# Kernel optimization log

Hardware: AMD Instinct MI355X
Metric: run time of the kernel (lower is better)

Reference implementation:

```python
import jax, jax.numpy as jnp
import numpy as np

B, C, H, W = 4, 256, 64, 64
CI = C // 2  # inter_channels


def setup_inputs() -> dict:
    key = jax.random.key(0)
    ks = jax.random.split(key, 10)
    s_in = 1.0 / np.sqrt(C)
    s_out = 1.0 / np.sqrt(CI)
    return {
        "rgbd": jax.random.normal(ks[0], (B, C, H, W), jnp.float32),
        "x": jax.random.normal(ks[1], (B, C, H, W), jnp.float32),
        "q_w": jax.random.uniform(ks[2], (CI, C), jnp.float32, -s_in, s_in),
        "q_b": jax.random.uniform(ks[3], (CI,), jnp.float32, -s_in, s_in),
        "k_w": jax.random.uniform(ks[4], (CI, C), jnp.float32, -s_in, s_in),
        "k_b": jax.random.uniform(ks[5], (CI,), jnp.float32, -s_in, s_in),
        "v_w": jax.random.uniform(ks[6], (CI, C), jnp.float32, -s_in, s_in),
        "v_b": jax.random.uniform(ks[7], (CI,), jnp.float32, -s_in, s_in),
        "out_w": jax.random.uniform(ks[8], (C, CI), jnp.float32, -s_out, s_out),
        "out_b": jax.random.uniform(ks[9], (C,), jnp.float32, -s_out, s_out),
    }


def reference(rgbd, x, q_w, q_b, k_w, k_b, v_w, v_b, out_w, out_b):
    b, c, h, w = rgbd.shape
    ci = q_w.shape[0]
    n = h * w
    # 1x1 convs == channel-wise linear maps; flatten spatial to tokens
    xs = x.reshape(b, c, n)        # [B, C, N]
    rs = rgbd.reshape(b, c, n)     # [B, C, N]
    q = jnp.einsum('oc,bcn->bno', q_w, xs) + q_b          # [B, N, CI]
    k = jnp.einsum('oc,bcn->bon', k_w, rs) + k_b[:, None]  # [B, CI, N]
    v = jnp.einsum('oc,bcn->bno', v_w, rs) + v_b          # [B, N, CI]
    attn = jax.nn.softmax(jnp.einsum('bqc,bck->bqk', q, k), axis=-1)  # [B, N, N]
    out = jnp.einsum('bqk,bkc->bqc', attn, v)             # [B, N, CI]
    out = jnp.einsum('oc,bnc->bon', out_w, out) + out_b[:, None]  # [B, C, N]
    return rgbd + out.reshape(b, c, h, w)
```

## Files before the change

### kernel.cpp

```cpp
#include <hip/hip_runtime.h>
#include <cstdint>
#include <cstddef>

typedef unsigned short u16;
typedef __attribute__((ext_vector_type(8))) short bf16x8;
typedef __attribute__((ext_vector_type(4))) float f32x4;
typedef __attribute__((ext_vector_type(16))) float f32x16;
typedef __attribute__((ext_vector_type(4))) uint32_t u32x4;

#define DEV __device__ __forceinline__

static constexpr float LOG2E = 1.4426950408889634f;

DEV u16 f2bf(float f) {
  uint32_t u = __float_as_uint(f);
  u += 0x7fffu + ((u >> 16) & 1u);
  return (u16)(u >> 16);
}
DEV float bf2f(u16 h) {
  uint32_t u = ((uint32_t)h) << 16;
  return __uint_as_float(u);
}
DEV uint32_t cvtpk(float lo, float hi) {
  uint32_t r;
  asm("v_cvt_pk_bf16_f32 %0, %1, %2" : "=v"(r) : "v"(lo), "v"(hi));
  return r;
}
DEV float exp2fast(float x) {
  float r;
  asm("v_exp_f32 %0, %1" : "=v"(r) : "v"(x));
  return r;
}
DEV void plswap(uint32_t& a, uint32_t& b) {
  asm("v_permlane32_swap_b32 %0, %1" : "+v"(a), "+v"(b));
}

DEV f32x4 mfma16(bf16x8 a, bf16x8 b, f32x4 c) {
  return __builtin_amdgcn_mfma_f32_16x16x32_bf16(a, b, c, 0, 0, 0);
}
DEV f32x16 mfma32(bf16x8 a, bf16x8 b, f32x16 c) {
  return __builtin_amdgcn_mfma_f32_32x32x16_bf16(a, b, c, 0, 0, 0);
}

DEV void gload_lds16(const void* g, void* l) {
  __builtin_amdgcn_global_load_lds(
      (const __attribute__((address_space(1))) uint32_t*)g,
      (__attribute__((address_space(3))) uint32_t*)l, 16, 0, 0);
}

static constexpr int BATCH = 4;
static constexpr int C = 256;
static constexpr int CI = 128;
static constexpr int N = 4096;
static constexpr int SPLIT = 4;

__global__ __launch_bounds__(256) void cvt_w(const float* __restrict__ a,
                                             const float* __restrict__ b,
                                             const float* __restrict__ c,
                                             const float* __restrict__ d,
                                             u16* __restrict__ oa, u16* __restrict__ ob,
                                             u16* __restrict__ oc, u16* __restrict__ od) {
  int i = blockIdx.x * 256 + threadIdx.x;
  oa[i] = f2bf(a[i] * LOG2E);
  ob[i] = f2bf(b[i]);
  oc[i] = f2bf(c[i]);
  od[i] = f2bf(d[i]);
}

__global__ __launch_bounds__(256) void proj_kernel(
    const float* __restrict__ x, const float* __restrict__ rgbd,
    const u16* __restrict__ Wq, const u16* __restrict__ Wk, const u16* __restrict__ Wv,
    const float* __restrict__ qb, const float* __restrict__ kb, const float* __restrict__ vb,
    u16* __restrict__ Qb, u16* __restrict__ Kb, u16* __restrict__ Vtb) {
  __shared__ __align__(16) u16 xT[64][C + 8];
  __shared__ __align__(16) u16 rT[64][C + 8];
  const int b = blockIdx.y;
  const int n0 = blockIdx.x * 64;
  const int t = threadIdx.x;
  {
    const int tok = t & 63, cp = (t >> 6) * 2;
    const float* xb = x + (size_t)b * C * N + n0;
    const float* rb = rgbd + (size_t)b * C * N + n0;
    for (int c0 = 0; c0 < C; c0 += 8) {
      int c = c0 + cp;
      *(uint32_t*)&xT[tok][c] = cvtpk(xb[(size_t)c * N + tok], xb[(size_t)(c + 1) * N + tok]);
      *(uint32_t*)&rT[tok][c] = cvtpk(rb[(size_t)c * N + tok], rb[(size_t)(c + 1) * N + tok]);
    }
  }
  __syncthreads();
  const int w = t >> 6, lane = t & 63, g = lane >> 4, cl = lane & 15;

#define PROJ_QK(Sarr, W, bias, Out, SCL)                                              \
  {                                                                                   \
    bf16x8 afr[8];                                                                    \
    _Pragma("unroll") for (int ks = 0; ks < 8; ++ks)                                  \
        afr[ks] = *(const bf16x8*)&Sarr[w * 16 + cl][ks * 32 + g * 8];                \
    _Pragma("unroll") for (int ct = 0; ct < 8; ++ct) {                                \
      f32x4 acc = {0.f, 0.f, 0.f, 0.f};                                               \
      _Pragma("unroll") for (int ks = 0; ks < 8; ++ks) {                              \
        bf16x8 bb = *(const bf16x8*)&W[(size_t)(ct * 16 + cl) * C + ks * 32 + g * 8]; \
        acc = mfma16(afr[ks], bb, acc);                                               \
      }                                                                               \
      float bv = bias[ct * 16 + cl] * (SCL);                                          \
      _Pragma("unroll") for (int r = 0; r < 4; ++r) {                                 \
        int tok = n0 + w * 16 + g * 4 + r;                                            \
        Out[((size_t)b * N + tok) * CI + ct * 16 + cl] = f2bf(acc[r] + bv);           \
      }                                                                               \
    }                                                                                 \
  }

  PROJ_QK(xT, Wq, qb, Qb, LOG2E)
  PROJ_QK(rT, Wk, kb, Kb, 1.0f)
#undef PROJ_QK

  #pragma unroll
  for (int rt = 0; rt < 2; ++rt) {
    bf16x8 aw[8];
    #pragma unroll
    for (int ks = 0; ks < 8; ++ks)
      aw[ks] = *(const bf16x8*)&Wv[(size_t)(w * 32 + rt * 16 + cl) * C + ks * 32 + g * 8];
    #pragma unroll
    for (int ct = 0; ct < 4; ++ct) {
      f32x4 acc = {0.f, 0.f, 0.f, 0.f};
      #pragma unroll
      for (int ks = 0; ks < 8; ++ks) {
        bf16x8 bb = *(const bf16x8*)&rT[ct * 16 + cl][ks * 32 + g * 8];
        acc = mfma16(aw[ks], bb, acc);
      }
      #pragma unroll
      for (int r = 0; r < 4; ++r) {
        int o = w * 32 + rt * 16 + g * 4 + r;
        Vtb[((size_t)b * CI + o) * N + n0 + ct * 16 + cl] = f2bf(acc[r] + vb[o]);
      }
    }
  }
}

template <int SPL>
__global__ __launch_bounds__(256, 2) void attn_kernel(
    const u16* __restrict__ Qb, const u16* __restrict__ Kb,
    const u16* __restrict__ Vtb, u16* __restrict__ Opart,
    float2* __restrict__ ml) {
  constexpr int KPB = N / SPL;
  constexpr int NT = KPB / 32;
  constexpr int CPX = 16 * SPL;
  __shared__ __align__(16) u16 Klds[2][32 * 128];
  __shared__ __align__(16) u16 Vlds[2][128 * 32];
  const int lin = blockIdx.x;
  const int nl = (lin & 7) * CPX + (lin >> 3);
  const int qi = nl & 31;
  const int grp = nl >> 5;
  const int b = grp & 3;
  const int s = grp >> 2;
  const int q0 = qi * 128;
  const int t = threadIdx.x;
  const int w = t >> 6, lane = t & 63;
  const int hi = lane >> 5, l31 = lane & 31;

  const u16* Kg = Kb + (size_t)b * N * CI;
  const u16* Vg = Vtb + (size_t)b * CI * N;

  const int k_r = t >> 4;
  const int k_ss = (t & 15) ^ k_r;
  const int v_r = t >> 2;
  const int v_ss = (t & 3) ^ ((t >> 3) & 3);
  const int wbase = (t & ~63);

#define STAGE_K(bi, k0_)                                                          \
  do {                                                                            \
    _Pragma("unroll") for (int c = 0; c < 2; ++c) {                               \
      gload_lds16(Kg + (size_t)((k0_) + c * 16 + k_r) * CI + k_ss * 8,            \
                  &Klds[bi][(c * 256 + wbase) * 8]);                              \
    }                                                                             \
  } while (0)
#define STAGE_V(bi, k0_)                                                          \
  do {                                                                            \
    _Pragma("unroll") for (int c = 0; c < 2; ++c) {                               \
      gload_lds16(Vg + (size_t)(c * 64 + v_r) * N + (k0_) + v_ss * 8,             \
                  &Vlds[bi][(c * 256 + wbase) * 8]);                              \
    }                                                                             \
  } while (0)

  const u16* Qg = Qb + ((size_t)b * N + q0 + w * 32 + l31) * CI;
  bf16x8 qf[8];
  #pragma unroll
  for (int mm = 0; mm < 8; ++mm)
    qf[mm] = *(const bf16x8*)(Qg + mm * 16 + hi * 8);
  asm volatile("s_waitcnt vmcnt(0)" ::: "memory");

  f32x16 oacc[4];
  #pragma unroll
  for (int ct = 0; ct < 4; ++ct)
    #pragma unroll
    for (int i = 0; i < 16; ++i) oacc[ct][i] = 0.f;
  float m_run = -1e30f, l_run = 0.f;

  const int kbeg = s * KPB;
  STAGE_K(0, kbeg);
  STAGE_V(0, kbeg);
  STAGE_K(1, kbeg + 32);
  STAGE_V(1, kbeg + 32);

  bf16x8 paA = {}, paB = {};
  bf16x8 vfp[4][2];

  int buf = 0;
  for (int tt = 0; tt < NT; ++tt) {
    asm volatile("s_waitcnt vmcnt(4)" ::: "memory");
    __builtin_amdgcn_s_barrier();
    const int knext = kbeg + ((tt + 2 < NT) ? tt + 2 : tt) * 32;

    bf16x8 kf[8];
    #pragma unroll
    for (int mm = 0; mm < 8; ++mm)
      kf[mm] = *(const bf16x8*)&Klds[buf][l31 * 128 + ((((mm << 1) | hi) ^ l31) & 15) * 8];
    asm volatile("s_waitcnt lgkmcnt(0)" ::: "memory");
    __builtin_amdgcn_sched_barrier(0);
    __builtin_amdgcn_s_barrier();
    STAGE_K(buf, knext);

    f32x16 st;
    #pragma unroll
    for (int i = 0; i < 16; ++i) st[i] = 0.f;
    __builtin_amdgcn_s_setprio(1);
    if (tt > 0) {
      #pragma unroll
      for (int ct = 0; ct < 4; ++ct) {
        oacc[ct] = mfma32(paA, vfp[ct][0], oacc[ct]);
        oacc[ct] = mfma32(paB, vfp[ct][1], oacc[ct]);
      }
    }
    #pragma unroll
    for (int mm = 0; mm < 8; ++mm) st = mfma32(kf[mm], qf[mm], st);
    __builtin_amdgcn_s_setprio(0);

    float tmax = st[0];
    #pragma unroll
    for (int i = 1; i < 16; ++i) tmax = fmaxf(tmax, st[i]);
    tmax = fmaxf(tmax, __shfl_xor(tmax, 32));
    if (!__all(tmax - m_run <= 11.5f)) {
      const float mn = fmaxf(m_run, tmax);
      const float alpha = exp2fast(m_run - mn);
      m_run = mn;
      l_run *= alpha;
      #pragma unroll
      for (int reg = 0; reg < 16; ++reg) {
        float ar = __shfl(alpha, (reg & 3) + 8 * (reg >> 2) + 4 * hi);
        oacc[0][reg] *= ar; oacc[1][reg] *= ar;
        oacc[2][reg] *= ar; oacc[3][reg] *= ar;
      }
    }
    float p[16];
    float ls = 0.f;
    #pragma unroll
    for (int i = 0; i < 16; ++i) {
      p[i] = exp2fast(st[i] - m_run);
      ls += p[i];
    }
    ls += __shfl_xor(ls, 32);
    l_run += ls;

    {
      uint32_t d0 = cvtpk(p[0], p[1]),   e0 = cvtpk(p[4], p[5]);
      uint32_t d1 = cvtpk(p[2], p[3]),   e1 = cvtpk(p[6], p[7]);
      uint32_t d2 = cvtpk(p[8], p[9]),   e2 = cvtpk(p[12], p[13]);
      uint32_t d3 = cvtpk(p[10], p[11]), e3 = cvtpk(p[14], p[15]);
      plswap(d0, e0);
      plswap(d1, e1);
      plswap(d2, e2);
      plswap(d3, e3);
      u32x4 pw0 = {d0, d1, e0, e1};
      u32x4 pw1 = {d2, d3, e2, e3};
      paA = __builtin_bit_cast(bf16x8, pw0);
      paB = __builtin_bit_cast(bf16x8, pw1);
    }

    const int vsw = (l31 >> 1) & 3;
    #pragma unroll
    for (int ct = 0; ct < 4; ++ct)
      #pragma unroll
      for (int ks = 0; ks < 2; ++ks)
        vfp[ct][ks] = *(const bf16x8*)
            &Vlds[buf][(32 * ct + l31) * 32 + ((((ks << 1) | hi) ^ vsw) & 3) * 8];
    asm volatile("s_waitcnt lgkmcnt(0)" ::: "memory");
    __builtin_amdgcn_sched_barrier(0);
    __builtin_amdgcn_s_barrier();
    STAGE_V(buf, knext);

    buf ^= 1;
  }
#undef STAGE_K
#undef STAGE_V

  __builtin_amdgcn_s_setprio(1);
  #pragma unroll
  for (int ct = 0; ct < 4; ++ct) {
    oacc[ct] = mfma32(paA, vfp[ct][0], oacc[ct]);
    oacc[ct] = mfma32(paB, vfp[ct][1], oacc[ct]);
  }
  __builtin_amdgcn_s_setprio(0);
  asm volatile("s_waitcnt vmcnt(0)" ::: "memory");

  const float inv = 1.0f / l_run;
  #pragma unroll
  for (int reg = 0; reg < 16; ++reg) {
    const int ql = (reg & 3) + 8 * (reg >> 2) + 4 * hi;
    const float invr = __shfl(inv, ql);
    const int q = q0 + w * 32 + ql;
    #pragma unroll
    for (int ct = 0; ct < 4; ++ct)
      Opart[(((size_t)(s * BATCH + b)) * N + q) * CI + 32 * ct + l31] =
          f2bf(oacc[ct][reg] * invr);
  }
  if (lane < 32) {
    const int q = q0 + w * 32 + lane;
    ml[(size_t)(s * BATCH + b) * N + q] = make_float2(m_run, l_run);
  }
}

__global__ __launch_bounds__(256) void outproj_kernel(
    const u16* __restrict__ Opart, const float2* __restrict__ ml,
    const u16* __restrict__ Wo, const float* __restrict__ obias,
    const float* __restrict__ rgbd, float* __restrict__ out) {
  __shared__ __align__(16) u16 ObL[64][CI + 8];
  const int b = blockIdx.y;
  const int n0 = blockIdx.x * 64;
  const int t = threadIdx.x;

  #pragma unroll
  for (int i = 0; i < 4; ++i) {
    const int idx = t + i * 256;
    const int row_l = idx >> 4, ci8 = idx & 15;
    const size_t row = (size_t)b * N + n0 + row_l;
    float2 sv[SPLIT];
    float M = -1e30f;
    #pragma unroll
    for (int sp = 0; sp < SPLIT; ++sp) {
      sv[sp] = ml[(size_t)sp * BATCH * N + row];
      M = fmaxf(M, sv[sp].x);
    }
    float wv[SPLIT], wsum = 0.f;
    #pragma unroll
    for (int sp = 0; sp < SPLIT; ++sp) {
      wv[sp] = sv[sp].y * exp2fast(sv[sp].x - M);
      wsum += wv[sp];
    }
    const float invL = 1.0f / wsum;
    float acc[8];
    #pragma unroll
    for (int j = 0; j < 8; ++j) acc[j] = 0.f;
    #pragma unroll
    for (int sp = 0; sp < SPLIT; ++sp) {
      const float wsc = wv[sp] * invL;
      bf16x8 v = *(const bf16x8*)&Opart[((size_t)sp * BATCH * N + row) * CI + ci8 * 8];
      #pragma unroll
      for (int j = 0; j < 8; ++j) acc[j] += wsc * bf2f((u16)v[j]);
    }
    bf16x8 o;
    #pragma unroll
    for (int j = 0; j < 8; ++j) o[j] = (short)f2bf(acc[j]);
    *(bf16x8*)&ObL[row_l][ci8 * 8] = o;
  }
  __syncthreads();

  const int w = t >> 6, lane = t & 63, g = lane >> 4, cl = lane & 15;
  f32x4 acc[4][4];
  #pragma unroll
  for (int i = 0; i < 4; ++i)
    #pragma unroll
    for (int j = 0; j < 4; ++j) acc[i][j] = {0.f, 0.f, 0.f, 0.f};

  #pragma unroll
  for (int ks = 0; ks < 4; ++ks) {
    bf16x8 bo[4];
    #pragma unroll
    for (int ct = 0; ct < 4; ++ct)
      bo[ct] = *(const bf16x8*)&ObL[ct * 16 + cl][ks * 32 + g * 8];
    #pragma unroll
    for (int rt = 0; rt < 4; ++rt) {
      bf16x8 aw = *(const bf16x8*)&Wo[(size_t)(w * 64 + rt * 16 + cl) * CI + ks * 32 + g * 8];
      #pragma unroll
      for (int ct = 0; ct < 4; ++ct) acc[rt][ct] = mfma16(aw, bo[ct], acc[rt][ct]);
    }
  }
  #pragma unroll
  for (int rt = 0; rt < 4; ++rt) {
    #pragma unroll
    for (int r = 0; r < 4; ++r) {
      const int o = w * 64 + rt * 16 + g * 4 + r;
      const float bb = obias[o];
      #pragma unroll
      for (int ct = 0; ct < 4; ++ct) {
        size_t idx = ((size_t)b * C + o) * N + n0 + ct * 16 + cl;
        out[idx] = rgbd[idx] + bb + acc[rt][ct][r];
      }
    }
  }
}

extern "C" void kernel_launch(void* const* d_in, const int* in_sizes, int n_in,
                              void* d_out, int out_size, void* d_ws, size_t ws_size,
                              hipStream_t stream) {
  (void)in_sizes; (void)n_in; (void)out_size; (void)ws_size;
  const float* rgbd = (const float*)d_in[0];
  const float* x    = (const float*)d_in[1];
  const float* q_w  = (const float*)d_in[2];
  const float* q_b  = (const float*)d_in[3];
  const float* k_w  = (const float*)d_in[4];
  const float* k_b  = (const float*)d_in[5];
  const float* v_w  = (const float*)d_in[6];
  const float* v_b  = (const float*)d_in[7];
  const float* o_w  = (const float*)d_in[8];
  const float* o_b  = (const float*)d_in[9];
  float* out = (float*)d_out;

  char* ws = (char*)d_ws;
  const size_t MB = 1024 * 1024;
  const size_t szQKV = (size_t)BATCH * N * CI * sizeof(u16);
  u16* Qb  = (u16*)(ws);
  u16* Kb  = (u16*)(ws + szQKV);
  u16* Vtb = (u16*)(ws + 2 * szQKV);
  u16* Wq  = (u16*)(ws + 3 * szQKV);
  u16* Wk  = Wq + (size_t)CI * C;
  u16* Wv  = Wk + (size_t)CI * C;
  u16* Wo  = Wv + (size_t)CI * C;
  u16* Opart = (u16*)(ws + 13 * MB);
  float2* ml = (float2*)(ws + 29 * MB);

  cvt_w<<<dim3((C * CI) / 256), 256, 0, stream>>>(q_w, k_w, v_w, o_w, Wq, Wk, Wv, Wo);
  proj_kernel<<<dim3(N / 64, BATCH), 256, 0, stream>>>(x, rgbd, Wq, Wk, Wv,
                                                       q_b, k_b, v_b, Qb, Kb, Vtb);
  attn_kernel<SPLIT><<<dim3(128 * SPLIT), 256, 0, stream>>>(Qb, Kb, Vtb, Opart, ml);
  outproj_kernel<<<dim3(N / 64, BATCH), 256, 0, stream>>>(Opart, ml, Wo, o_b, rgbd, out);
}
```

Baseline: 89.66 us.

## Shrink attention blocks to 64 queries and merge K/V staging into one barrier

The attention kernel now uses 128-thread blocks covering 64 query rows each, so it launches twice as many blocks. K and V tiles are staged together with one barrier per iteration. The software-pipelined PV MFMA, which used the previous tile's probabilities, is replaced by an in-iteration PV step. This is meant to improve occupancy and load balance and to remove a barrier. The cost is that each K/V tile is loaded by twice as many blocks, and the overlap between the softmax and the PV MFMAs is lost.

After: 93.81 us. 4.6% more time.

```diff
diff --git a/kernel.cpp b/kernel.cpp
--- a/kernel.cpp
+++ b/kernel.cpp
@@ -137,22 +137,22 @@
 }
 
 template <int SPL>
-__global__ __launch_bounds__(256, 2) void attn_kernel(
+__global__ __launch_bounds__(128, 2) void attn_kernel(
     const u16* __restrict__ Qb, const u16* __restrict__ Kb,
     const u16* __restrict__ Vtb, u16* __restrict__ Opart,
     float2* __restrict__ ml) {
   constexpr int KPB = N / SPL;
   constexpr int NT = KPB / 32;
-  constexpr int CPX = 16 * SPL;
+  constexpr int CPX = 32 * SPL;
   __shared__ __align__(16) u16 Klds[2][32 * 128];
   __shared__ __align__(16) u16 Vlds[2][128 * 32];
   const int lin = blockIdx.x;
   const int nl = (lin & 7) * CPX + (lin >> 3);
-  const int qi = nl & 31;
-  const int grp = nl >> 5;
+  const int qi = nl & 63;
+  const int grp = nl >> 6;
   const int b = grp & 3;
   const int s = grp >> 2;
-  const int q0 = qi * 128;
+  const int q0 = qi * 64;
   const int t = threadIdx.x;
   const int w = t >> 6, lane = t & 63;
   const int hi = lane >> 5, l31 = lane & 31;
@@ -160,24 +160,21 @@
   const u16* Kg = Kb + (size_t)b * N * CI;
   const u16* Vg = Vtb + (size_t)b * CI * N;
 
-  const int k_r = t >> 4;
-  const int k_ss = (t & 15) ^ k_r;
-  const int v_r = t >> 2;
   const int v_ss = (t & 3) ^ ((t >> 3) & 3);
   const int wbase = (t & ~63);
 
-#define STAGE_K(bi, k0_)                                                          \
+#define STAGE_KV(bi, k0_)                                                         \
   do {                                                                            \
-    _Pragma("unroll") for (int c = 0; c < 2; ++c) {                               \
-      gload_lds16(Kg + (size_t)((k0_) + c * 16 + k_r) * CI + k_ss * 8,            \
-                  &Klds[bi][(c * 256 + wbase) * 8]);                              \
+    _Pragma("unroll") for (int c = 0; c < 4; ++c) {                               \
+      const int r = c * 8 + (t >> 4);                                             \
+      const int ss = (t & 15) ^ (r & 15);                                         \
+      gload_lds16(Kg + (size_t)((k0_) + r) * CI + ss * 8,                         \
+                  &Klds[bi][(c * 128 + wbase) * 8]);                              \
     }                                                                             \
-  } while (0)
-#define STAGE_V(bi, k0_)                                                          \
-  do {                                                                            \
-    _Pragma("unroll") for (int c = 0; c < 2; ++c) {                               \
-      gload_lds16(Vg + (size_t)(c * 64 + v_r) * N + (k0_) + v_ss * 8,             \
-                  &Vlds[bi][(c * 256 + wbase) * 8]);                              \
+    _Pragma("unroll") for (int c = 0; c < 4; ++c) {                               \
+      const int vr = c * 32 + (t >> 2);                                           \
+      gload_lds16(Vg + (size_t)vr * N + (k0_) + v_ss * 8,                         \
+                  &Vlds[bi][(c * 128 + wbase) * 8]);                              \
     }                                                                             \
   } while (0)
 
@@ -196,17 +193,12 @@
   float m_run = -1e30f, l_run = 0.f;
 
   const int kbeg = s * KPB;
-  STAGE_K(0, kbeg);
-  STAGE_V(0, kbeg);
-  STAGE_K(1, kbeg + 32);
-  STAGE_V(1, kbeg + 32);
-
-  bf16x8 paA = {}, paB = {};
-  bf16x8 vfp[4][2];
+  STAGE_KV(0, kbeg);
+  STAGE_KV(1, kbeg + 32);
 
   int buf = 0;
   for (int tt = 0; tt < NT; ++tt) {
-    asm volatile("s_waitcnt vmcnt(4)" ::: "memory");
+    asm volatile("s_waitcnt vmcnt(8)" ::: "memory");
     __builtin_amdgcn_s_barrier();
     const int knext = kbeg + ((tt + 2 < NT) ? tt + 2 : tt) * 32;
 
@@ -214,22 +206,23 @@
     #pragma unroll
     for (int mm = 0; mm < 8; ++mm)
       kf[mm] = *(const bf16x8*)&Klds[buf][l31 * 128 + ((((mm << 1) | hi) ^ l31) & 15) * 8];
+    bf16x8 vf[4][2];
+    const int vsw = (l31 >> 1) & 3;
+    #pragma unroll
+    for (int ct = 0; ct < 4; ++ct)
+      #pragma unroll
+      for (int ks = 0; ks < 2; ++ks)
+        vf[ct][ks] = *(const bf16x8*)
+            &Vlds[buf][(32 * ct + l31) * 32 + ((((ks << 1) | hi) ^ vsw) & 3) * 8];
     asm volatile("s_waitcnt lgkmcnt(0)" ::: "memory");
     __builtin_amdgcn_sched_barrier(0);
     __builtin_amdgcn_s_barrier();
-    STAGE_K(buf, knext);
+    STAGE_KV(buf, knext);
 
     f32x16 st;
     #pragma unroll
     for (int i = 0; i < 16; ++i) st[i] = 0.f;
     __builtin_amdgcn_s_setprio(1);
-    if (tt > 0) {
-      #pragma unroll
-      for (int ct = 0; ct < 4; ++ct) {
-        oacc[ct] = mfma32(paA, vfp[ct][0], oacc[ct]);
-        oacc[ct] = mfma32(paB, vfp[ct][1], oacc[ct]);
-      }
-    }
     #pragma unroll
     for (int mm = 0; mm < 8; ++mm) st = mfma32(kf[mm], qf[mm], st);
     __builtin_amdgcn_s_setprio(0);
@@ -260,45 +253,30 @@
     ls += __shfl_xor(ls, 32);
     l_run += ls;
 
-    {
-      uint32_t d0 = cvtpk(p[0], p[1]),   e0 = cvtpk(p[4], p[5]);
-      uint32_t d1 = cvtpk(p[2], p[3]),   e1 = cvtpk(p[6], p[7]);
-      uint32_t d2 = cvtpk(p[8], p[9]),   e2 = cvtpk(p[12], p[13]);
-      uint32_t d3 = cvtpk(p[10], p[11]), e3 = cvtpk(p[14], p[15]);
-      plswap(d0, e0);
-      plswap(d1, e1);
-      plswap(d2, e2);
-      plswap(d3, e3);
-      u32x4 pw0 = {d0, d1, e0, e1};
-      u32x4 pw1 = {d2, d3, e2, e3};
-      paA = __builtin_bit_cast(bf16x8, pw0);
-      paB = __builtin_bit_cast(bf16x8, pw1);
-    }
-
-    const int vsw = (l31 >> 1) & 3;
-    #pragma unroll
-    for (int ct = 0; ct < 4; ++ct)
-      #pragma unroll
-      for (int ks = 0; ks < 2; ++ks)
-        vfp[ct][ks] = *(const bf16x8*)
-            &Vlds[buf][(32 * ct + l31) * 32 + ((((ks << 1) | hi) ^ vsw) & 3) * 8];
-    asm volatile("s_waitcnt lgkmcnt(0)" ::: "memory");
-    __builtin_amdgcn_sched_barrier(0);
-    __builtin_amdgcn_s_barrier();
-    STAGE_V(buf, knext);
+    uint32_t d0 = cvtpk(p[0], p[1]),   e0 = cvtpk(p[4], p[5]);
+    uint32_t d1 = cvtpk(p[2], p[3]),   e1 = cvtpk(p[6], p[7]);
+    uint32_t d2 = cvtpk(p[8], p[9]),   e2 = cvtpk(p[12], p[13]);
+    uint32_t d3 = cvtpk(p[10], p[11]), e3 = cvtpk(p[14], p[15]);
+    plswap(d0, e0);
+    plswap(d1, e1);
+    plswap(d2, e2);
+    plswap(d3, e3);
+    u32x4 pw0 = {d0, d1, e0, e1};
+    u32x4 pw1 = {d2, d3, e2, e3};
+    bf16x8 pa0 = __builtin_bit_cast(bf16x8, pw0);
+    bf16x8 pa1 = __builtin_bit_cast(bf16x8, pw1);
+
+    __builtin_amdgcn_s_setprio(1);
+    #pragma unroll
+    for (int ct = 0; ct < 4; ++ct) {
+      oacc[ct] = mfma32(pa0, vf[ct][0], oacc[ct]);
+      oacc[ct] = mfma32(pa1, vf[ct][1], oacc[ct]);
+    }
+    __builtin_amdgcn_s_setprio(0);
 
     buf ^= 1;
   }
-#undef STAGE_K
-#undef STAGE_V
-
-  __builtin_amdgcn_s_setprio(1);
-  #pragma unroll
-  for (int ct = 0; ct < 4; ++ct) {
-    oacc[ct] = mfma32(paA, vfp[ct][0], oacc[ct]);
-    oacc[ct] = mfma32(paB, vfp[ct][1], oacc[ct]);
-  }
-  __builtin_amdgcn_s_setprio(0);
+#undef STAGE_KV
   asm volatile("s_waitcnt vmcnt(0)" ::: "memory");
 
   const float inv = 1.0f / l_run;
@@ -430,6 +408,6 @@
   cvt_w<<<dim3((C * CI) / 256), 256, 0, stream>>>(q_w, k_w, v_w, o_w, Wq, Wk, Wv, Wo);
   proj_kernel<<<dim3(N / 64, BATCH), 256, 0, stream>>>(x, rgbd, Wq, Wk, Wv,
                                                        q_b, k_b, v_b, Qb, Kb, Vtb);
-  attn_kernel<SPLIT><<<dim3(128 * SPLIT), 256, 0, stream>>>(Qb, Kb, Vtb, Opart, ml);
+  attn_kernel<SPLIT><<<dim3(64 * BATCH * SPLIT), 128, 0, stream>>>(Qb, Kb, Vtb, Opart, ml);
   outproj_kernel<<<dim3(N / 64, BATCH), 256, 0, stream>>>(Opart, ml, Wo, o_b, rgbd, out);
 }
```
